# Kernel tuning notes

Hardware: AMD Instinct MI355X
Metric: run time of the kernel (lower is better)

Reference implementation:

```python
import jax, jax.numpy as jnp
import numpy as np

N, D_IN, D_OUT, E = 100000, 64, 64, 1600000


def setup_inputs() -> dict:
    key = jax.random.key(0)
    k1, k2, k3, k4, k5 = jax.random.split(key, 5)
    x = jax.random.normal(k1, (N, D_IN), dtype=jnp.float32)
    edge_index = jax.random.randint(k2, (2, E), 0, N, dtype=jnp.int64)
    # Linear params (PyTorch default: uniform(-1/sqrt(fan_in), 1/sqrt(fan_in)))
    bound = 1.0 / np.sqrt(D_IN)
    W_self = jax.random.uniform(k3, (D_IN, D_OUT), jnp.float32, -bound, bound)
    b_self = jnp.zeros((D_OUT,), jnp.float32)
    W_neigh = jax.random.uniform(k4, (D_IN, D_OUT), jnp.float32, -bound, bound)
    b_neigh = jax.random.uniform(k5, (D_OUT,), jnp.float32, -bound, bound)
    return {"x": x, "edge_index": edge_index, "W_self": W_self,
            "b_self": b_self, "W_neigh": W_neigh, "b_neigh": b_neigh}


def reference(x, edge_index, W_self, b_self, W_neigh, b_neigh):
    src, dst = edge_index[0], edge_index[1]
    # gather messages from source nodes, scatter-add into destinations
    agg = jax.ops.segment_sum(x[src], dst, num_segments=x.shape[0])  # [N, D_IN]
    # in-degree, clamped to >= 1 (matches bincount().clamp_min(1))
    deg = jax.ops.segment_sum(jnp.ones_like(dst, dtype=x.dtype), dst,
                              num_segments=x.shape[0])
    deg = jnp.maximum(deg, 1.0)[:, None]
    agg = agg / deg
    h = x @ W_self + b_self + agg @ W_neigh + b_neigh
    # dropout is identity in eval mode
    return jax.nn.relu(h)
```

## Files before the change

kernel.cpp:

```cpp
#include <hip/hip_runtime.h>


#define D 64
#define CVTB 1024
#define WTB 4
#define NB 782
#define BKN 128
#define REGC 2560
#define KP 136

typedef __attribute__((ext_vector_type(8))) short bf8_t;
typedef __attribute__((ext_vector_type(4))) float f4_t;

__device__ inline unsigned int bf_rn(float f) {
  unsigned int u = __float_as_uint(f);
  return (u + 0x7FFFu + ((u >> 16) & 1u)) >> 16;
}
__device__ inline unsigned int packbf2(float a, float b) {
  return bf_rn(a) | (bf_rn(b) << 16);
}

__global__ __launch_bounds__(256) void pre_k(const float* __restrict__ x,
                                             unsigned short* __restrict__ xbf,
                                             int total4,
                                             int* __restrict__ pcur,
                                             const float* __restrict__ Ws,
                                             const float* __restrict__ Wn,
                                             const float* __restrict__ bs,
                                             const float* __restrict__ bn,
                                             unsigned short* __restrict__ wtbf,
                                             float* __restrict__ biasf) {
  int p = blockIdx.x;
  int t = threadIdx.x;
  if (p < CVTB) {
    int i = p * 256 + t;
    int stride = CVTB * 256;
    for (; i < total4; i += stride) {
      float4 v = ((const float4*)x)[i];
      uint2 r;
      r.x = packbf2(v.x, v.y);
      r.y = packbf2(v.z, v.w);
      ((uint2*)xbf)[i] = r;
    }
  } else if (p == CVTB) {
    for (int i = t; i < NB; i += 256) pcur[i] = 0;
  } else {
    int idx = (p - CVTB - 1) * 256 + t;
    int j = idx >> 4, kq = idx & 15, k0 = kq * 8;
    float v[8];
#pragma unroll
    for (int u = 0; u < 8; u++) {
      int k = k0 + u;
      v[u] = (k < 64) ? Ws[k * 64 + j] : Wn[(k - 64) * 64 + j];
    }
    uint4 r;
    r.x = packbf2(v[0], v[1]);
    r.y = packbf2(v[2], v[3]);
    r.z = packbf2(v[4], v[5]);
    r.w = packbf2(v[6], v[7]);
    *(uint4*)&wtbf[j * 128 + k0] = r;
    if (idx < 64) biasf[idx] = bs[idx] + bn[idx];
  }
}

__global__ __launch_bounds__(256) void part_k(const int* __restrict__ ei,
                                              int* __restrict__ parts,
                                              int* __restrict__ pcur,
                                              int E, int chunk) {
  __shared__ int h[NB];
  __shared__ int base[NB];
  int p = blockIdx.x;
  int t = threadIdx.x;
  for (int i = t; i < NB; i += 256) h[i] = 0;
  __syncthreads();
  int s = p * chunk, e = min(E, s + chunk);
  int n4 = (e - s) >> 2;
  const int4* s4 = (const int4*)(ei + s);
  const int4* d4 = (const int4*)(ei + E + s);
  for (int i = t; i < n4; i += 256) {
    int4 dv = d4[i];
    atomicAdd(&h[dv.x >> 7], 1);
    atomicAdd(&h[dv.y >> 7], 1);
    atomicAdd(&h[dv.z >> 7], 1);
    atomicAdd(&h[dv.w >> 7], 1);
  }
  for (int i = s + (n4 << 2) + t; i < e; i += 256)
    atomicAdd(&h[ei[E + i] >> 7], 1);
  __syncthreads();
  for (int i = t; i < NB; i += 256) {
    int c = h[i];
    base[i] = (c > 0) ? atomicAdd(&pcur[i], c) : 0;
    h[i] = 0;
  }
  __syncthreads();
  for (int i = t; i < n4; i += 256) {
    int4 sv = s4[i];
    int4 dv = d4[i];
    int b, r, pos;
    b = dv.x >> 7; r = atomicAdd(&h[b], 1); pos = base[b] + r;
    if (pos < REGC) parts[b * REGC + pos] = (sv.x << 7) | (dv.x & 127);
    b = dv.y >> 7; r = atomicAdd(&h[b], 1); pos = base[b] + r;
    if (pos < REGC) parts[b * REGC + pos] = (sv.y << 7) | (dv.y & 127);
    b = dv.z >> 7; r = atomicAdd(&h[b], 1); pos = base[b] + r;
    if (pos < REGC) parts[b * REGC + pos] = (sv.z << 7) | (dv.z & 127);
    b = dv.w >> 7; r = atomicAdd(&h[b], 1); pos = base[b] + r;
    if (pos < REGC) parts[b * REGC + pos] = (sv.w << 7) | (dv.w & 127);
  }
  for (int i = s + (n4 << 2) + t; i < e; i += 256) {
    int sv = ei[i], dd = ei[E + i];
    int b = dd >> 7;
    int r = atomicAdd(&h[b], 1);
    int pos = base[b] + r;
    if (pos < REGC) parts[b * REGC + pos] = (sv << 7) | (dd & 127);
  }
}

__global__ __launch_bounds__(512) void k_bagg(const unsigned short* __restrict__ xbf,
                                              const int* __restrict__ parts,
                                              const int* __restrict__ pcur,
                                              unsigned short* __restrict__ aggbf,
                                              int N) {
  __shared__ int stage[REGC];
  __shared__ int sorted[REGC];
  __shared__ int cnt[BKN];
  __shared__ int off[BKN];
  __shared__ int cur[BKN];
  __shared__ int wtot[2];
  int b = blockIdx.x;
  int t = threadIdx.x;
  if (t < BKN) cnt[t] = 0;
  __syncthreads();
  int ce = pcur[b];
  if (ce > REGC) ce = REGC;
  const int* pb = parts + b * REGC;
  for (int i = t; i < ce; i += 512) {
    int v = pb[i];
    stage[i] = v;
    atomicAdd(&cnt[v & 127], 1);
  }
  __syncthreads();
  int lane = t & 63, w = t >> 6;
  int v0 = 0, inc = 0;
  if (t < BKN) {
    v0 = cnt[t];
    inc = v0;
    for (int o = 1; o < 64; o <<= 1) {
      int u = __shfl_up(inc, o, 64);
      if (lane >= o) inc += u;
    }
    if (lane == 63) wtot[w] = inc;
  }
  __syncthreads();
  if (t < BKN) {
    int e0 = inc - v0 + (w ? wtot[0] : 0);
    off[t] = e0;
    cur[t] = e0;
  }
  __syncthreads();
  for (int i = t; i < ce; i += 512) {
    int v = stage[i];
    int pos = atomicAdd(&cur[v & 127], 1);
    sorted[pos] = v & 0x7FFFFF80;
  }
  __syncthreads();
  int grp = t >> 3, fg = t & 7;
  const char* xb = (const char*)xbf;
  int n0 = b * BKN;
#pragma unroll
  for (int it = 0; it < 2; it++) {
    int dl = it * 64 + grp;
    int n = n0 + dl;
    int deg = cnt[dl];
    int st = off[dl], en = st + deg;
    f4_t e0 = {0.f, 0.f, 0.f, 0.f}, o0 = {0.f, 0.f, 0.f, 0.f};
    f4_t e1 = {0.f, 0.f, 0.f, 0.f}, o1 = {0.f, 0.f, 0.f, 0.f};
    int i = st;
    for (; i + 4 <= en; i += 4) {
      int a0 = sorted[i], a1 = sorted[i + 1];
      int a2 = sorted[i + 2], a3 = sorted[i + 3];
      uint4 u0 = *(const uint4*)(xb + a0 + fg * 16);
      uint4 u1 = *(const uint4*)(xb + a1 + fg * 16);
      uint4 u2 = *(const uint4*)(xb + a2 + fg * 16);
      uint4 u3 = *(const uint4*)(xb + a3 + fg * 16);
      f4_t pe, po;
      pe.x = __uint_as_float(u0.x << 16); pe.y = __uint_as_float(u0.y << 16);
      pe.z = __uint_as_float(u0.z << 16); pe.w = __uint_as_float(u0.w << 16);
      po.x = __uint_as_float(u0.x & 0xFFFF0000u); po.y = __uint_as_float(u0.y & 0xFFFF0000u);
      po.z = __uint_as_float(u0.z & 0xFFFF0000u); po.w = __uint_as_float(u0.w & 0xFFFF0000u);
      e0 += pe; o0 += po;
      pe.x = __uint_as_float(u1.x << 16); pe.y = __uint_as_float(u1.y << 16);
      pe.z = __uint_as_float(u1.z << 16); pe.w = __uint_as_float(u1.w << 16);
      po.x = __uint_as_float(u1.x & 0xFFFF0000u); po.y = __uint_as_float(u1.y & 0xFFFF0000u);
      po.z = __uint_as_float(u1.z & 0xFFFF0000u); po.w = __uint_as_float(u1.w & 0xFFFF0000u);
      e1 += pe; o1 += po;
      pe.x = __uint_as_float(u2.x << 16); pe.y = __uint_as_float(u2.y << 16);
      pe.z = __uint_as_float(u2.z << 16); pe.w = __uint_as_float(u2.w << 16);
      po.x = __uint_as_float(u2.x & 0xFFFF0000u); po.y = __uint_as_float(u2.y & 0xFFFF0000u);
      po.z = __uint_as_float(u2.z & 0xFFFF0000u); po.w = __uint_as_float(u2.w & 0xFFFF0000u);
      e0 += pe; o0 += po;
      pe.x = __uint_as_float(u3.x << 16); pe.y = __uint_as_float(u3.y << 16);
      pe.z = __uint_as_float(u3.z << 16); pe.w = __uint_as_float(u3.w << 16);
      po.x = __uint_as_float(u3.x & 0xFFFF0000u); po.y = __uint_as_float(u3.y & 0xFFFF0000u);
      po.z = __uint_as_float(u3.z & 0xFFFF0000u); po.w = __uint_as_float(u3.w & 0xFFFF0000u);
      e1 += pe; o1 += po;
    }
    for (; i < en; i++) {
      int a0 = sorted[i];
      uint4 u0 = *(const uint4*)(xb + a0 + fg * 16);
      f4_t pe, po;
      pe.x = __uint_as_float(u0.x << 16); pe.y = __uint_as_float(u0.y << 16);
      pe.z = __uint_as_float(u0.z << 16); pe.w = __uint_as_float(u0.w << 16);
      po.x = __uint_as_float(u0.x & 0xFFFF0000u); po.y = __uint_as_float(u0.y & 0xFFFF0000u);
      po.z = __uint_as_float(u0.z & 0xFFFF0000u); po.w = __uint_as_float(u0.w & 0xFFFF0000u);
      e0 += pe; o0 += po;
    }
    e0 += e1; o0 += o1;
    float inv = 1.f / (float)(deg > 0 ? deg : 1);
    if (n < N) {
      uint4 r;
      r.x = packbf2(e0.x * inv, o0.x * inv);
      r.y = packbf2(e0.y * inv, o0.y * inv);
      r.z = packbf2(e0.z * inv, o0.z * inv);
      r.w = packbf2(e0.w * inv, o0.w * inv);
      *(uint4*)(aggbf + (size_t)n * D + fg * 8) = r;
    }
  }
}

__global__ __launch_bounds__(256) void k_gemm(const unsigned short* __restrict__ xbf,
                                              const unsigned short* __restrict__ aggbf,
                                              const unsigned short* __restrict__ wtbf,
                                              const float* __restrict__ biasf,
                                              float* __restrict__ out, int ntiles) {
  __shared__ unsigned short sWT[64 * KP];
  __shared__ unsigned short sA[4 * 16 * KP];

  int t = threadIdx.x;
#pragma unroll
  for (int i = 0; i < 4; i++) {
    int idx = i * 256 + t;
    int row = idx >> 4, q = idx & 15;
    *(uint4*)&sWT[row * KP + q * 8] = *(const uint4*)&wtbf[row * 128 + q * 8];
  }
  __syncthreads();

  int w = t >> 6, lane = t & 63;
  int row = lane & 15, part = lane >> 4;
  unsigned short* myA = &sA[w * 16 * KP];

  for (int tile = blockIdx.x * 4 + w; tile < ntiles; tile += gridDim.x * 4) {
    int n0 = tile * 16;
    {
      const unsigned short* srcp =
          (part < 2) ? (xbf + (size_t)(n0 + row) * D + (part & 1) * 32)
                     : (aggbf + (size_t)(n0 + row) * D + (part & 1) * 32);
      const uint4* s4 = (const uint4*)srcp;
      uint4* d4 = (uint4*)&myA[row * KP + part * 32];
      d4[0] = s4[0];
      d4[1] = s4[1];
      d4[2] = s4[2];
      d4[3] = s4[3];
    }
    bf8_t af[4];
#pragma unroll
    for (int kt = 0; kt < 4; kt++)
      af[kt] = *(const bf8_t*)&myA[row * KP + kt * 32 + part * 8];
#pragma unroll
    for (int jt = 0; jt < 4; jt++) {
      f4_t acc = {0.f, 0.f, 0.f, 0.f};
#pragma unroll
      for (int kt = 0; kt < 4; kt++) {
        bf8_t bfr = *(const bf8_t*)&sWT[(jt * 16 + row) * KP + kt * 32 + part * 8];
        acc = __builtin_amdgcn_mfma_f32_16x16x32_bf16(af[kt], bfr, acc, 0, 0, 0);
      }
      int col = jt * 16 + row;
      float bias = biasf[col];
#pragma unroll
      for (int r = 0; r < 4; r++) {
        float v = acc[r] + bias;
        v = v > 0.f ? v : 0.f;
        out[(size_t)(n0 + part * 4 + r) * D + col] = v;
      }
    }
  }
}

extern "C" void kernel_launch(void* const* d_in, const int* in_sizes, int n_in,
                              void* d_out, int out_size, void* d_ws, size_t ws_size,
                              hipStream_t stream) {
  const float* x      = (const float*)d_in[0];
  const int*   ei     = (const int*)d_in[1];
  const float* Wself  = (const float*)d_in[2];
  const float* bself  = (const float*)d_in[3];
  const float* Wneigh = (const float*)d_in[4];
  const float* bneigh = (const float*)d_in[5];

  int N = in_sizes[0] / D;
  int E = in_sizes[1] / 2;
  int ntiles = (N + 15) / 16;
  int chunk = (((E + 255) / 256) + 3) & ~3;

  unsigned short* xbf   = (unsigned short*)d_ws;
  unsigned short* aggbf = xbf + (size_t)N * D;
  unsigned short* wtbf  = aggbf + (size_t)N * D;
  float* biasf    = (float*)(wtbf + 64 * 128);
  int* pcur       = (int*)(biasf + 64);
  int* parts      = pcur + ((NB + 3) & ~3);

  pre_k<<<CVTB + 1 + WTB, 256, 0, stream>>>(x, xbf, N * D / 4, pcur,
                                            Wself, Wneigh, bself, bneigh,
                                            wtbf, biasf);
  part_k<<<256, 256, 0, stream>>>(ei, parts, pcur, E, chunk);
  k_bagg<<<NB, 512, 0, stream>>>(xbf, parts, pcur, aggbf, N);
  k_gemm<<<782, 256, 0, stream>>>(xbf, aggbf, wtbf, biasf, (float*)d_out, ntiles);
}
```

Baseline: 148.9 us.

## Fuse aggregation with GEMM and merge partition into conversion kernel

Merges edge partitioning, x-to-bf16 conversion and weight packing into one prep kernel, and replaces the pcur zeroing block with a memset. The aggregation kernel now also runs the MFMA GEMM on its 128 destination rows, keeping the aggregated bf16 rows in swizzled LDS, so the agg buffer is never written to or read back from global memory. The staging copy of partition entries is dropped in favour of reading them from global twice. This removes a launch and a global round trip, but the fused kernel uses more LDS per block, and the merged prep kernel may run partitioning alongside conversion.

```diff
diff --git a/kernel.cpp b/kernel.cpp
--- a/kernel.cpp
+++ b/kernel.cpp
@@ -2,12 +2,14 @@
 
 
 #define D 64
+#define PARTB 256
 #define CVTB 1024
 #define WTB 4
 #define NB 782
 #define BKN 128
 #define REGC 2560
 #define KP 136
+#define SORTB (REGC * 4)
 
 typedef __attribute__((ext_vector_type(8))) short bf8_t;
 typedef __attribute__((ext_vector_type(4))) float f4_t;
@@ -20,20 +22,68 @@
   return bf_rn(a) | (bf_rn(b) << 16);
 }
 
-__global__ __launch_bounds__(256) void pre_k(const float* __restrict__ x,
-                                             unsigned short* __restrict__ xbf,
-                                             int total4,
-                                             int* __restrict__ pcur,
-                                             const float* __restrict__ Ws,
-                                             const float* __restrict__ Wn,
-                                             const float* __restrict__ bs,
-                                             const float* __restrict__ bn,
-                                             unsigned short* __restrict__ wtbf,
-                                             float* __restrict__ biasf) {
+__global__ __launch_bounds__(256) void prep_k(const int* __restrict__ ei,
+                                              int* __restrict__ parts,
+                                              int* __restrict__ pcur,
+                                              int E, int chunk,
+                                              const float* __restrict__ x,
+                                              unsigned short* __restrict__ xbf,
+                                              int total4,
+                                              const float* __restrict__ Ws,
+                                              const float* __restrict__ Wn,
+                                              const float* __restrict__ bs,
+                                              const float* __restrict__ bn,
+                                              unsigned short* __restrict__ wtbf,
+                                              float* __restrict__ biasf) {
+  __shared__ int h[NB];
+  __shared__ int base[NB];
   int p = blockIdx.x;
   int t = threadIdx.x;
-  if (p < CVTB) {
-    int i = p * 256 + t;
+  if (p < PARTB) {
+    for (int i = t; i < NB; i += 256) h[i] = 0;
+    __syncthreads();
+    int s = p * chunk, e = min(E, s + chunk);
+    int n4 = (e - s) >> 2;
+    const int4* s4 = (const int4*)(ei + s);
+    const int4* d4 = (const int4*)(ei + E + s);
+    for (int i = t; i < n4; i += 256) {
+      int4 dv = d4[i];
+      atomicAdd(&h[dv.x >> 7], 1);
+      atomicAdd(&h[dv.y >> 7], 1);
+      atomicAdd(&h[dv.z >> 7], 1);
+      atomicAdd(&h[dv.w >> 7], 1);
+    }
+    for (int i = s + (n4 << 2) + t; i < e; i += 256)
+      atomicAdd(&h[ei[E + i] >> 7], 1);
+    __syncthreads();
+    for (int i = t; i < NB; i += 256) {
+      int c = h[i];
+      base[i] = (c > 0) ? atomicAdd(&pcur[i], c) : 0;
+      h[i] = 0;
+    }
+    __syncthreads();
+    for (int i = t; i < n4; i += 256) {
+      int4 sv = s4[i];
+      int4 dv = d4[i];
+      int b, r, pos;
+      b = dv.x >> 7; r = atomicAdd(&h[b], 1); pos = base[b] + r;
+      if (pos < REGC) parts[b * REGC + pos] = (sv.x << 7) | (dv.x & 127);
+      b = dv.y >> 7; r = atomicAdd(&h[b], 1); pos = base[b] + r;
+      if (pos < REGC) parts[b * REGC + pos] = (sv.y << 7) | (dv.y & 127);
+      b = dv.z >> 7; r = atomicAdd(&h[b], 1); pos = base[b] + r;
+      if (pos < REGC) parts[b * REGC + pos] = (sv.z << 7) | (dv.z & 127);
+      b = dv.w >> 7; r = atomicAdd(&h[b], 1); pos = base[b] + r;
+      if (pos < REGC) parts[b * REGC + pos] = (sv.w << 7) | (dv.w & 127);
+    }
+    for (int i = s + (n4 << 2) + t; i < e; i += 256) {
+      int sv = ei[i], dd = ei[E + i];
+      int b = dd >> 7;
+      int r = atomicAdd(&h[b], 1);
+      int pos = base[b] + r;
+      if (pos < REGC) parts[b * REGC + pos] = (sv << 7) | (dd & 127);
+    }
+  } else if (p < PARTB + CVTB) {
+    int i = (p - PARTB) * 256 + t;
     int stride = CVTB * 256;
     for (; i < total4; i += stride) {
       float4 v = ((const float4*)x)[i];
@@ -42,10 +92,8 @@
       r.y = packbf2(v.z, v.w);
       ((uint2*)xbf)[i] = r;
     }
-  } else if (p == CVTB) {
-    for (int i = t; i < NB; i += 256) pcur[i] = 0;
   } else {
-    int idx = (p - CVTB - 1) * 256 + t;
+    int idx = (p - PARTB - CVTB) * 256 + t;
     int j = idx >> 4, kq = idx & 15, k0 = kq * 8;
     float v[8];
 #pragma unroll
@@ -63,83 +111,37 @@
   }
 }
 
-__global__ __launch_bounds__(256) void part_k(const int* __restrict__ ei,
-                                              int* __restrict__ parts,
-                                              int* __restrict__ pcur,
-                                              int E, int chunk) {
-  __shared__ int h[NB];
-  __shared__ int base[NB];
-  int p = blockIdx.x;
-  int t = threadIdx.x;
-  for (int i = t; i < NB; i += 256) h[i] = 0;
-  __syncthreads();
-  int s = p * chunk, e = min(E, s + chunk);
-  int n4 = (e - s) >> 2;
-  const int4* s4 = (const int4*)(ei + s);
-  const int4* d4 = (const int4*)(ei + E + s);
-  for (int i = t; i < n4; i += 256) {
-    int4 dv = d4[i];
-    atomicAdd(&h[dv.x >> 7], 1);
-    atomicAdd(&h[dv.y >> 7], 1);
-    atomicAdd(&h[dv.z >> 7], 1);
-    atomicAdd(&h[dv.w >> 7], 1);
-  }
-  for (int i = s + (n4 << 2) + t; i < e; i += 256)
-    atomicAdd(&h[ei[E + i] >> 7], 1);
-  __syncthreads();
-  for (int i = t; i < NB; i += 256) {
-    int c = h[i];
-    base[i] = (c > 0) ? atomicAdd(&pcur[i], c) : 0;
-    h[i] = 0;
-  }
-  __syncthreads();
-  for (int i = t; i < n4; i += 256) {
-    int4 sv = s4[i];
-    int4 dv = d4[i];
-    int b, r, pos;
-    b = dv.x >> 7; r = atomicAdd(&h[b], 1); pos = base[b] + r;
-    if (pos < REGC) parts[b * REGC + pos] = (sv.x << 7) | (dv.x & 127);
-    b = dv.y >> 7; r = atomicAdd(&h[b], 1); pos = base[b] + r;
-    if (pos < REGC) parts[b * REGC + pos] = (sv.y << 7) | (dv.y & 127);
-    b = dv.z >> 7; r = atomicAdd(&h[b], 1); pos = base[b] + r;
-    if (pos < REGC) parts[b * REGC + pos] = (sv.z << 7) | (dv.z & 127);
-    b = dv.w >> 7; r = atomicAdd(&h[b], 1); pos = base[b] + r;
-    if (pos < REGC) parts[b * REGC + pos] = (sv.w << 7) | (dv.w & 127);
-  }
-  for (int i = s + (n4 << 2) + t; i < e; i += 256) {
-    int sv = ei[i], dd = ei[E + i];
-    int b = dd >> 7;
-    int r = atomicAdd(&h[b], 1);
-    int pos = base[b] + r;
-    if (pos < REGC) parts[b * REGC + pos] = (sv << 7) | (dd & 127);
-  }
-}
-
-__global__ __launch_bounds__(512) void k_bagg(const unsigned short* __restrict__ xbf,
+__global__ __launch_bounds__(512) void k_fuse(const unsigned short* __restrict__ xbf,
                                               const int* __restrict__ parts,
                                               const int* __restrict__ pcur,
-                                              unsigned short* __restrict__ aggbf,
-                                              int N) {
-  __shared__ int stage[REGC];
-  __shared__ int sorted[REGC];
-  __shared__ int cnt[BKN];
-  __shared__ int off[BKN];
-  __shared__ int cur[BKN];
+                                              const unsigned short* __restrict__ wtbf,
+                                              const float* __restrict__ biasf,
+                                              float* __restrict__ out, int N) {
+  __shared__ unsigned short sWT[64 * KP];
+  __shared__ __align__(16) unsigned char dyn[16384];
   __shared__ int wtot[2];
+  int* sorted = (int*)dyn;
+  int* cnt = (int*)(dyn + SORTB);
+  int* off = cnt + BKN;
+  int* cur = off + BKN;
+
   int b = blockIdx.x;
   int t = threadIdx.x;
+#pragma unroll
+  for (int i = 0; i < 2; i++) {
+    int idx = i * 512 + t;
+    int row = idx >> 4, q = idx & 15;
+    *(uint4*)&sWT[row * KP + q * 8] = *(const uint4*)&wtbf[row * 128 + q * 8];
+  }
   if (t < BKN) cnt[t] = 0;
   __syncthreads();
+
   int ce = pcur[b];
   if (ce > REGC) ce = REGC;
   const int* pb = parts + b * REGC;
-  for (int i = t; i < ce; i += 512) {
-    int v = pb[i];
-    stage[i] = v;
-    atomicAdd(&cnt[v & 127], 1);
-  }
-  __syncthreads();
-  int lane = t & 63, w = t >> 6;
+  for (int i = t; i < ce; i += 512) atomicAdd(&cnt[pb[i] & 127], 1);
+  __syncthreads();
+  int lane = t & 63, w2 = t >> 6;
   int v0 = 0, inc = 0;
   if (t < BKN) {
     v0 = cnt[t];
@@ -148,28 +150,28 @@
       int u = __shfl_up(inc, o, 64);
       if (lane >= o) inc += u;
     }
-    if (lane == 63) wtot[w] = inc;
+    if (lane == 63) wtot[w2] = inc;
   }
   __syncthreads();
   if (t < BKN) {
-    int e0 = inc - v0 + (w ? wtot[0] : 0);
+    int e0 = inc - v0 + (w2 ? wtot[0] : 0);
     off[t] = e0;
     cur[t] = e0;
   }
   __syncthreads();
   for (int i = t; i < ce; i += 512) {
-    int v = stage[i];
+    int v = pb[i];
     int pos = atomicAdd(&cur[v & 127], 1);
     sorted[pos] = v & 0x7FFFFF80;
   }
   __syncthreads();
+
   int grp = t >> 3, fg = t & 7;
   const char* xb = (const char*)xbf;
-  int n0 = b * BKN;
+  uint4 res[2];
 #pragma unroll
   for (int it = 0; it < 2; it++) {
     int dl = it * 64 + grp;
-    int n = n0 + dl;
     int deg = cnt[dl];
     int st = off[dl], en = st + deg;
     f4_t e0 = {0.f, 0.f, 0.f, 0.f}, o0 = {0.f, 0.f, 0.f, 0.f};
@@ -216,70 +218,44 @@
     }
     e0 += e1; o0 += o1;
     float inv = 1.f / (float)(deg > 0 ? deg : 1);
-    if (n < N) {
-      uint4 r;
-      r.x = packbf2(e0.x * inv, o0.x * inv);
-      r.y = packbf2(e0.y * inv, o0.y * inv);
-      r.z = packbf2(e0.z * inv, o0.z * inv);
-      r.w = packbf2(e0.w * inv, o0.w * inv);
-      *(uint4*)(aggbf + (size_t)n * D + fg * 8) = r;
-    }
-  }
-}
-
-__global__ __launch_bounds__(256) void k_gemm(const unsigned short* __restrict__ xbf,
-                                              const unsigned short* __restrict__ aggbf,
-                                              const unsigned short* __restrict__ wtbf,
-                                              const float* __restrict__ biasf,
-                                              float* __restrict__ out, int ntiles) {
-  __shared__ unsigned short sWT[64 * KP];
-  __shared__ unsigned short sA[4 * 16 * KP];
-
-  int t = threadIdx.x;
-#pragma unroll
-  for (int i = 0; i < 4; i++) {
-    int idx = i * 256 + t;
-    int row = idx >> 4, q = idx & 15;
-    *(uint4*)&sWT[row * KP + q * 8] = *(const uint4*)&wtbf[row * 128 + q * 8];
-  }
-  __syncthreads();
-
-  int w = t >> 6, lane = t & 63;
+    res[it].x = packbf2(e0.x * inv, o0.x * inv);
+    res[it].y = packbf2(e0.y * inv, o0.y * inv);
+    res[it].z = packbf2(e0.z * inv, o0.z * inv);
+    res[it].w = packbf2(e0.w * inv, o0.w * inv);
+  }
+  __syncthreads();
+#pragma unroll
+  for (int it = 0; it < 2; it++) {
+    int dl = it * 64 + grp;
+    *(uint4*)(dyn + dl * 128 + ((fg * 16) ^ ((dl & 7) << 4))) = res[it];
+  }
+  __syncthreads();
+
+  int w = t >> 6;
   int row = lane & 15, part = lane >> 4;
-  unsigned short* myA = &sA[w * 16 * KP];
-
-  for (int tile = blockIdx.x * 4 + w; tile < ntiles; tile += gridDim.x * 4) {
-    int n0 = tile * 16;
-    {
-      const unsigned short* srcp =
-          (part < 2) ? (xbf + (size_t)(n0 + row) * D + (part & 1) * 32)
-                     : (aggbf + (size_t)(n0 + row) * D + (part & 1) * 32);
-      const uint4* s4 = (const uint4*)srcp;
-      uint4* d4 = (uint4*)&myA[row * KP + part * 32];
-      d4[0] = s4[0];
-      d4[1] = s4[1];
-      d4[2] = s4[2];
-      d4[3] = s4[3];
-    }
-    bf8_t af[4];
-#pragma unroll
-    for (int kt = 0; kt < 4; kt++)
-      af[kt] = *(const bf8_t*)&myA[row * KP + kt * 32 + part * 8];
+  int rtile = w * 16;
+  int n0g = b * BKN + rtile;
+  if (n0g < N) {
+    int r = rtile + row;
+    bf8_t af0 = *(const bf8_t*)&xbf[(size_t)(n0g + row) * D + part * 8];
+    bf8_t af1 = *(const bf8_t*)&xbf[(size_t)(n0g + row) * D + 32 + part * 8];
+    bf8_t af2 = *(const bf8_t*)(dyn + r * 128 + ((part * 16) ^ ((r & 7) << 4)));
+    bf8_t af3 = *(const bf8_t*)(dyn + r * 128 + ((64 + part * 16) ^ ((r & 7) << 4)));
 #pragma unroll
     for (int jt = 0; jt < 4; jt++) {
       f4_t acc = {0.f, 0.f, 0.f, 0.f};
-#pragma unroll
-      for (int kt = 0; kt < 4; kt++) {
-        bf8_t bfr = *(const bf8_t*)&sWT[(jt * 16 + row) * KP + kt * 32 + part * 8];
-        acc = __builtin_amdgcn_mfma_f32_16x16x32_bf16(af[kt], bfr, acc, 0, 0, 0);
-      }
+      const unsigned short* wrow = &sWT[(jt * 16 + row) * KP + part * 8];
+      acc = __builtin_amdgcn_mfma_f32_16x16x32_bf16(af0, *(const bf8_t*)&wrow[0], acc, 0, 0, 0);
+      acc = __builtin_amdgcn_mfma_f32_16x16x32_bf16(af1, *(const bf8_t*)&wrow[32], acc, 0, 0, 0);
+      acc = __builtin_amdgcn_mfma_f32_16x16x32_bf16(af2, *(const bf8_t*)&wrow[64], acc, 0, 0, 0);
+      acc = __builtin_amdgcn_mfma_f32_16x16x32_bf16(af3, *(const bf8_t*)&wrow[96], acc, 0, 0, 0);
       int col = jt * 16 + row;
       float bias = biasf[col];
 #pragma unroll
-      for (int r = 0; r < 4; r++) {
-        float v = acc[r] + bias;
+      for (int rr = 0; rr < 4; rr++) {
+        float v = acc[rr] + bias;
         v = v > 0.f ? v : 0.f;
-        out[(size_t)(n0 + part * 4 + r) * D + col] = v;
+        out[(size_t)(n0g + part * 4 + rr) * D + col] = v;
       }
     }
   }
@@ -297,20 +273,19 @@
 
   int N = in_sizes[0] / D;
   int E = in_sizes[1] / 2;
-  int ntiles = (N + 15) / 16;
-  int chunk = (((E + 255) / 256) + 3) & ~3;
-
-  unsigned short* xbf   = (unsigned short*)d_ws;
-  unsigned short* aggbf = xbf + (size_t)N * D;
-  unsigned short* wtbf  = aggbf + (size_t)N * D;
-  float* biasf    = (float*)(wtbf + 64 * 128);
-  int* pcur       = (int*)(biasf + 64);
-  int* parts      = pcur + ((NB + 3) & ~3);
-
-  pre_k<<<CVTB + 1 + WTB, 256, 0, stream>>>(x, xbf, N * D / 4, pcur,
-                                            Wself, Wneigh, bself, bneigh,
-                                            wtbf, biasf);
-  part_k<<<256, 256, 0, stream>>>(ei, parts, pcur, E, chunk);
-  k_bagg<<<NB, 512, 0, stream>>>(xbf, parts, pcur, aggbf, N);
-  k_gemm<<<782, 256, 0, stream>>>(xbf, aggbf, wtbf, biasf, (float*)d_out, ntiles);
-}
+  int chunk = (((E + PARTB - 1) / PARTB) + 3) & ~3;
+
+  unsigned short* xbf  = (unsigned short*)d_ws;
+  unsigned short* wtbf = xbf + (size_t)N * D;
+  float* biasf   = (float*)(wtbf + 64 * 128);
+  int* pcur      = (int*)(biasf + 64);
+  int* parts     = pcur + ((NB + 3) & ~3);
+
+  hipMemsetAsync(pcur, 0, NB * sizeof(int), stream);
+  prep_k<<<PARTB + CVTB + WTB, 256, 0, stream>>>(ei, parts, pcur, E, chunk,
+                                                 x, xbf, N * D / 4,
+                                                 Wself, Wneigh, bself, bneigh,
+                                                 wtbf, biasf);
+  k_fuse<<<NB, 512, 0, stream>>>(xbf, parts, pcur, wtbf, biasf,
+                                 (float*)d_out, N);
+}
```

Result: faster. 142.6 us, median of 2 (-4.2%).
